# Performance work log

Hardware: AMD Instinct MI355X
Metric: run time of the kernel (lower is better)

## Reference

```python
import jax, jax.numpy as jnp
import numpy as np

M = 2          # interp_dim
D = 4          # interp_degree
MESH_LOWER = np.array([0.0, 0.0], dtype=np.float32)
MESH_UPPER = np.array([1.0, 1.0], dtype=np.float32)
MESH_SIZE = np.array([64, 64], dtype=np.int32)   # coe grid = mesh_size*D+1 = [257, 257]


def _lagrange_basis(t):
    """t: [N, M] local coordinate in [0, D]; returns bases [N, M, D+1].
    L_j(t) = prod_{k != j} (t - k) / (j - k)."""
    ks = jnp.arange(D + 1, dtype=t.dtype)
    tk = t[..., None] - ks                       # [N, M, D+1]
    bs = []
    for j in range(D + 1):                       # small fixed loop over D+1=5 bases
        num = jnp.ones(t.shape, t.dtype)
        denom = 1.0
        for k in range(D + 1):
            if k != j:
                num = num * tk[..., k]
                denom *= float(j - k)
        bs.append(num / denom)
    return jnp.stack(bs, axis=-1)                # [N, M, D+1]


def setup_inputs() -> dict:
    key = jax.random.key(0)
    k1, k2 = jax.random.split(key)
    inputs = jax.random.uniform(k1, (2048, 2048, M), dtype=jnp.float32)  # points in [0,1)^2
    grid = tuple(int(s) * D + 1 for s in MESH_SIZE)                      # (257, 257)
    interp_coe = jax.random.normal(k2, grid, dtype=jnp.float32)
    return {"inputs": inputs, "interp_coe": interp_coe}


def reference(inputs, interp_coe):
    size = inputs.shape
    x = inputs.reshape(-1, M)                                   # [N, M]
    lower = jnp.asarray(MESH_LOWER, x.dtype)
    upper = jnp.asarray(MESH_UPPER, x.dtype)
    msize = jnp.asarray(MESH_SIZE.astype(np.float32), x.dtype)
    u = (x - lower) / (upper - lower) * msize                   # grid coordinates
    cell = jnp.clip(jnp.floor(u), 0.0, msize - 1.0)             # [N, M] element index
    t = (u - cell) * D                                          # local coord in [0, D]
    basis = _lagrange_basis(t)                                  # [N, M, D+1]
    base = cell.astype(jnp.int32) * D                           # [N, M] global node base index
    offs = jnp.arange(D + 1, dtype=jnp.int32)
    i0 = base[:, 0, None] + offs                                # [N, D+1]
    i1 = base[:, 1, None] + offs                                # [N, D+1]
    coe = interp_coe[i0[:, :, None], i1[:, None, :]]            # [N, D+1, D+1] gathered cell coes
    out = jnp.einsum('nij,ni,nj->n', coe, basis[:, 0], basis[:, 1])
    return out.reshape(size[:-1])
```

## Files before the change

### kernel.cpp

```cpp
#include <hip/hip_runtime.h>

#define NGRID 257
#define LDS_PITCH 260
#define LDS_BYTES (LDS_PITCH * NGRID * 2)
#define BLOCK 1024
#define GRID 256
#define ITERS 16

typedef _Float16 half2_t __attribute__((ext_vector_type(2)));
typedef _Float16 half4_t __attribute__((ext_vector_type(4)));

struct __attribute__((packed, aligned(4))) f4u { float x, y, z, w; };

struct PtFrag {
    half4_t lo[5];
    half2_t hi[5];
};

__device__ __forceinline__ void lag_basis(float t, float b[5]) {
    float f0 = t;
    float f1 = t - 1.0f;
    float f2 = t - 2.0f;
    float f3 = t - 3.0f;
    float f4 = t - 4.0f;
    float p01 = f0 * f1;
    float p12 = f1 * f2;
    float p23 = f2 * f3;
    float p34 = f3 * f4;
    b[0] = p12 * p34 * (1.0f / 24.0f);
    b[1] = f0 * f2 * p34 * (-1.0f / 6.0f);
    b[2] = p01 * p34 * (1.0f / 4.0f);
    b[3] = p01 * f2 * f4 * (-1.0f / 6.0f);
    b[4] = p01 * p23 * (1.0f / 24.0f);
}

__device__ __forceinline__ int pt_off(float x0, float x1) {
    float u0 = x0 * 64.0f, u1 = x1 * 64.0f;
    float c0 = fminf(fmaxf(floorf(u0), 0.0f), 63.0f);
    float c1 = fminf(fmaxf(floorf(u1), 0.0f), 63.0f);
    return ((int)c0 * 4) * LDS_PITCH + ((int)c1 * 4);
}

__device__ __forceinline__ void stage_point(const _Float16* __restrict__ lds,
                                            int off, PtFrag& f) {
    const _Float16* base = lds + off;
#pragma unroll
    for (int i = 0; i < 5; ++i)
        f.lo[i] = *(const half4_t*)(base + i * LDS_PITCH);
#pragma unroll
    for (int i = 0; i < 5; ++i)
        f.hi[i] = *(const half2_t*)(base + i * LDS_PITCH + 4);
}

__device__ __forceinline__ float eval_pt(const PtFrag& f, float x0, float x1) {
    float u0 = x0 * 64.0f, u1 = x1 * 64.0f;
    float c0 = fminf(fmaxf(floorf(u0), 0.0f), 63.0f);
    float c1 = fminf(fmaxf(floorf(u1), 0.0f), 63.0f);
    float b0[5], b1[5];
    lag_basis((u0 - c0) * 4.0f, b0);
    lag_basis((u1 - c1) * 4.0f, b1);
    float acc = 0.0f;
#pragma unroll
    for (int i = 0; i < 5; ++i) {
        float rd = (float)f.lo[i][0] * b1[0];
        rd = fmaf((float)f.lo[i][1], b1[1], rd);
        rd = fmaf((float)f.lo[i][2], b1[2], rd);
        rd = fmaf((float)f.lo[i][3], b1[3], rd);
        rd = fmaf((float)f.hi[i][0], b1[4], rd);
        acc = fmaf(b0[i], rd, acc);
    }
    return acc;
}

__launch_bounds__(BLOCK, 4)
__global__ void lagrange_kernel(const float* __restrict__ inputs,
                                const float* __restrict__ coe,
                                float* __restrict__ out,
                                int npts) {
    extern __shared__ _Float16 lds[];

    for (int g = threadIdx.x; g < NGRID * 65; g += BLOCK) {
        int r = g / 65;
        int c4 = (g - r * 65) * 4;
        if (c4 < 256) {
            f4u q = *(const f4u*)(coe + r * NGRID + c4);
            half4_t h = { (_Float16)q.x, (_Float16)q.y,
                          (_Float16)q.z, (_Float16)q.w };
            *(half4_t*)(lds + r * LDS_PITCH + c4) = h;
        } else {
            lds[r * LDS_PITCH + 256] = (_Float16)coe[r * NGRID + 256];
        }
    }
    __syncthreads();

    const float2* __restrict__ in2 = (const float2*)inputs;
    const int tid = blockIdx.x * BLOCK + threadIdx.x;
    const int stride = GRID * BLOCK;
    (void)npts;

    float2 w0, w1, w2, w3;
    PtFrag f[3];

    w0 = in2[tid];
    w1 = in2[tid + stride];
    w2 = in2[tid + 2 * stride];
    stage_point(lds, pt_off(w0.x, w0.y), f[0]);
    stage_point(lds, pt_off(w1.x, w1.y), f[1]);

#pragma unroll
    for (int k = 0; k < ITERS; ++k) {
        if (k + 3 < ITERS) w3 = in2[tid + (k + 3) * stride];
        if (k + 2 < ITERS) stage_point(lds, pt_off(w2.x, w2.y), f[(k + 2) % 3]);
        float r = eval_pt(f[k % 3], w0.x, w0.y);
        __builtin_nontemporal_store(r, &out[tid + k * stride]);
        w0 = w1;
        w1 = w2;
        w2 = w3;
    }
}

extern "C" void kernel_launch(void* const* d_in, const int* in_sizes, int n_in,
                              void* d_out, int out_size, void* d_ws, size_t ws_size,
                              hipStream_t stream) {
    const float* inputs = (const float*)d_in[0];
    const float* coe    = (const float*)d_in[1];
    float* out = (float*)d_out;
    int npts = out_size;

    (void)hipFuncSetAttribute((const void*)lagrange_kernel,
                              hipFuncAttributeMaxDynamicSharedMemorySize,
                              LDS_BYTES);

    dim3 grid(GRID), block(BLOCK);
    hipLaunchKernelGGL(lagrange_kernel, grid, block, LDS_BYTES, stream,
                       inputs, coe, out, npts);
}
```

Measured before the change: 94.82 us.

## Split coefficient table across block pairs to halve LDS and raise occupancy

Each pair of blocks now covers the same contiguous chunk of points, and each block stages only half of the coefficient rows (129 rows) into LDS. Every block reads all points in its chunk and evaluates only those whose cell row falls in its half. The smaller LDS footprint and launch bound of 8 are meant to allow more resident waves, and the software-pipelined staging of coefficients into registers is removed in favour of direct LDS reads. In exchange, every input point is loaded twice, half the lanes sit idle on each iteration, and the nontemporal stores become ordinary stores.

```diff
diff --git a/kernel.cpp b/kernel.cpp
--- a/kernel.cpp
+++ b/kernel.cpp
@@ -2,20 +2,16 @@
 
 #define NGRID 257
 #define LDS_PITCH 260
-#define LDS_BYTES (LDS_PITCH * NGRID * 2)
+#define LDS_ROWS 129
+#define LDS_BYTES (LDS_PITCH * LDS_ROWS * 2)
 #define BLOCK 1024
-#define GRID 256
+#define GRID 512
 #define ITERS 16
 
 typedef _Float16 half2_t __attribute__((ext_vector_type(2)));
 typedef _Float16 half4_t __attribute__((ext_vector_type(4)));
 
 struct __attribute__((packed, aligned(4))) f4u { float x, y, z, w; };
-
-struct PtFrag {
-    half4_t lo[5];
-    half2_t hi[5];
-};
 
 __device__ __forceinline__ void lag_basis(float t, float b[5]) {
     float f0 = t;
@@ -34,88 +30,74 @@
     b[4] = p01 * p23 * (1.0f / 24.0f);
 }
 
-__device__ __forceinline__ int pt_off(float x0, float x1) {
-    float u0 = x0 * 64.0f, u1 = x1 * 64.0f;
-    float c0 = fminf(fmaxf(floorf(u0), 0.0f), 63.0f);
-    float c1 = fminf(fmaxf(floorf(u1), 0.0f), 63.0f);
-    return ((int)c0 * 4) * LDS_PITCH + ((int)c1 * 4);
-}
-
-__device__ __forceinline__ void stage_point(const _Float16* __restrict__ lds,
-                                            int off, PtFrag& f) {
-    const _Float16* base = lds + off;
-#pragma unroll
-    for (int i = 0; i < 5; ++i)
-        f.lo[i] = *(const half4_t*)(base + i * LDS_PITCH);
-#pragma unroll
-    for (int i = 0; i < 5; ++i)
-        f.hi[i] = *(const half2_t*)(base + i * LDS_PITCH + 4);
-}
-
-__device__ __forceinline__ float eval_pt(const PtFrag& f, float x0, float x1) {
-    float u0 = x0 * 64.0f, u1 = x1 * 64.0f;
-    float c0 = fminf(fmaxf(floorf(u0), 0.0f), 63.0f);
-    float c1 = fminf(fmaxf(floorf(u1), 0.0f), 63.0f);
+__device__ __forceinline__ float eval_pt(const _Float16* __restrict__ lds,
+                                         int row_base, int col_base,
+                                         float t0, float t1) {
     float b0[5], b1[5];
-    lag_basis((u0 - c0) * 4.0f, b0);
-    lag_basis((u1 - c1) * 4.0f, b1);
+    lag_basis(t0, b0);
+    lag_basis(t1, b1);
+    int off = row_base * LDS_PITCH + col_base;
     float acc = 0.0f;
 #pragma unroll
     for (int i = 0; i < 5; ++i) {
-        float rd = (float)f.lo[i][0] * b1[0];
-        rd = fmaf((float)f.lo[i][1], b1[1], rd);
-        rd = fmaf((float)f.lo[i][2], b1[2], rd);
-        rd = fmaf((float)f.lo[i][3], b1[3], rd);
-        rd = fmaf((float)f.hi[i][0], b1[4], rd);
+        const _Float16* rp = lds + off + i * LDS_PITCH;
+        half4_t lo = *(const half4_t*)rp;
+        _Float16 e4 = rp[4];
+        float rd = (float)lo[0] * b1[0];
+        rd = fmaf((float)lo[1], b1[1], rd);
+        rd = fmaf((float)lo[2], b1[2], rd);
+        rd = fmaf((float)lo[3], b1[3], rd);
+        rd = fmaf((float)e4, b1[4], rd);
         acc = fmaf(b0[i], rd, acc);
     }
     return acc;
 }
 
-__launch_bounds__(BLOCK, 4)
+__launch_bounds__(BLOCK, 8)
 __global__ void lagrange_kernel(const float* __restrict__ inputs,
                                 const float* __restrict__ coe,
                                 float* __restrict__ out,
                                 int npts) {
     extern __shared__ _Float16 lds[];
 
-    for (int g = threadIdx.x; g < NGRID * 65; g += BLOCK) {
+    const int j    = blockIdx.x >> 1;
+    const int half = blockIdx.x & 1;
+    const int row0 = half * 128;
+
+    for (int g = threadIdx.x; g < LDS_ROWS * 65; g += BLOCK) {
         int r = g / 65;
         int c4 = (g - r * 65) * 4;
+        const float* src = coe + (r + row0) * NGRID;
         if (c4 < 256) {
-            f4u q = *(const f4u*)(coe + r * NGRID + c4);
+            f4u q = *(const f4u*)(src + c4);
             half4_t h = { (_Float16)q.x, (_Float16)q.y,
                           (_Float16)q.z, (_Float16)q.w };
             *(half4_t*)(lds + r * LDS_PITCH + c4) = h;
         } else {
-            lds[r * LDS_PITCH + 256] = (_Float16)coe[r * NGRID + 256];
+            lds[r * LDS_PITCH + 256] = (_Float16)src[256];
         }
     }
     __syncthreads();
 
     const float2* __restrict__ in2 = (const float2*)inputs;
-    const int tid = blockIdx.x * BLOCK + threadIdx.x;
-    const int stride = GRID * BLOCK;
+    const int base = j * (BLOCK * ITERS) + threadIdx.x;
     (void)npts;
-
-    float2 w0, w1, w2, w3;
-    PtFrag f[3];
-
-    w0 = in2[tid];
-    w1 = in2[tid + stride];
-    w2 = in2[tid + 2 * stride];
-    stage_point(lds, pt_off(w0.x, w0.y), f[0]);
-    stage_point(lds, pt_off(w1.x, w1.y), f[1]);
 
 #pragma unroll
     for (int k = 0; k < ITERS; ++k) {
-        if (k + 3 < ITERS) w3 = in2[tid + (k + 3) * stride];
-        if (k + 2 < ITERS) stage_point(lds, pt_off(w2.x, w2.y), f[(k + 2) % 3]);
-        float r = eval_pt(f[k % 3], w0.x, w0.y);
-        __builtin_nontemporal_store(r, &out[tid + k * stride]);
-        w0 = w1;
-        w1 = w2;
-        w2 = w3;
+        int idx = base + k * BLOCK;
+        float2 w = in2[idx];
+        float u0 = w.x * 64.0f, u1 = w.y * 64.0f;
+        float c0 = fminf(fmaxf(floorf(u0), 0.0f), 63.0f);
+        float c1 = fminf(fmaxf(floorf(u1), 0.0f), 63.0f);
+        int ic0 = (int)c0;
+        if ((ic0 >> 5) == half) {
+            int row_base = ic0 * 4 - row0;
+            int col_base = (int)c1 * 4;
+            float r = eval_pt(lds, row_base, col_base,
+                              (u0 - c0) * 4.0f, (u1 - c1) * 4.0f);
+            out[idx] = r;
+        }
     }
 }
 
```

Result: slower. 101.8 us (+7.4%).
